# Kernel optimization log

Measured on AMD Instinct MI355X. Metric: run time of the kernel, lower is better.

Reference implementation:

```python
import jax, jax.numpy as jnp
import numpy as np

N = [40000, 10000, 2500, 625, 157]  # vertex counts per mesh level (0 = full res)
K = 6


def _propagate(x, row, col, norm, n):
    # x: [B, N_in, C]; gather neighbor feats, weight by norm, scatter-add to rows
    msg = x[:, col, :] * norm[None, :, None]          # [B, E, C]
    return jnp.zeros((x.shape[0], n, x.shape[2]), x.dtype).at[:, row, :].add(msg)


def cheb_conv(x, edge_index, W, b, n):
    # Chebyshev graph conv with sym-normalized adjacency (lambda_max=2 / CoMA convention)
    row, col = edge_index[0], edge_index[1]
    deg = jnp.zeros((n,), x.dtype).at[row].add(jnp.ones(row.shape, x.dtype))
    dinv = jnp.where(deg > 0, deg ** -0.5, jnp.zeros_like(deg))
    norm = dinv[row] * dinv[col]
    Tx0 = x
    out = jnp.einsum('bnc,cd->bnd', Tx0, W[0])
    Tx1 = _propagate(Tx0, row, col, norm, n)
    out = out + jnp.einsum('bnc,cd->bnd', Tx1, W[1])
    for k in range(2, W.shape[0]):
        Tx2 = 2.0 * _propagate(Tx1, row, col, norm, n) - Tx0
        out = out + jnp.einsum('bnc,cd->bnd', Tx2, W[k])
        Tx0, Tx1 = Tx1, Tx2
    return out + b


def pool(x, row, col, val, n_out):
    # sparse COO upsampling: out[:, row] += val * x[:, col]  (Pool() in torch source)
    msg = x[:, col, :] * val[None, :, None]
    return jnp.zeros((x.shape[0], n_out, x.shape[2]), x.dtype).at[:, row, :].add(msg)


def setup_inputs() -> dict:
    key = jax.random.key(0)
    ks = iter(jax.random.split(key, 64))
    B, latent = 16, 128
    inp = {}
    inp['x'] = jax.random.normal(next(ks), (B, latent), jnp.float32)
    inp['lin_w'] = jax.random.normal(next(ks), (latent, N[4] * 64), jnp.float32) * 0.05
    inp['lin_b'] = jnp.zeros((N[4] * 64,), jnp.float32)
    for i in range(4):
        inp[f'edge{i}'] = jax.random.randint(next(ks), (2, 6 * N[i]), 0, N[i])
    for i in range(4):
        nnz = 3 * N[i]
        inp[f'up{i}_row'] = jax.random.randint(next(ks), (nnz,), 0, N[i])
        inp[f'up{i}_col'] = jax.random.randint(next(ks), (nnz,), 0, N[i + 1])
        inp[f'up{i}_val'] = jax.random.uniform(next(ks), (nnz,), jnp.float32)
    # Deblock Cheb weights: (in,out) = (64,64),(64,32),(32,32),(32,32); final (32,3)
    for j, (ci, co) in enumerate([(64, 64), (64, 32), (32, 32), (32, 32)], start=1):
        inp[f'W{j}'] = jax.random.normal(next(ks), (K, ci, co), jnp.float32) * 0.05
        inp[f'b{j}'] = jnp.zeros((co,), jnp.float32)
    inp['Wout'] = jax.random.normal(next(ks), (K, 32, 3), jnp.float32) * 0.05
    inp['bout'] = jnp.zeros((3,), jnp.float32)
    return inp


def reference(x, lin_w, lin_b, edge0, edge1, edge2, edge3,
              up0_row, up0_col, up0_val, up1_row, up1_col, up1_val,
              up2_row, up2_col, up2_val, up3_row, up3_col, up3_val,
              W1, b1, W2, b2, W3, b3, W4, b4, Wout, bout):
    B = x.shape[0]
    h = (x @ lin_w + lin_b).reshape(B, N[4], 64)        # latent -> coarsest mesh
    edges = [edge0, edge1, edge2, edge3]
    ups = [(up0_row, up0_col, up0_val), (up1_row, up1_col, up1_val),
           (up2_row, up2_col, up2_val), (up3_row, up3_col, up3_val)]
    Ws = [(W1, b1), (W2, b2), (W3, b3), (W4, b4)]
    for j in range(4):
        lvl = 3 - j  # deblock j upsamples to mesh level lvl (coarse -> fine)
        row, col, val = ups[lvl]
        h = pool(h, row, col, val, N[lvl])
        h = jax.nn.elu(cheb_conv(h, edges[lvl], Ws[j][0], Ws[j][1], N[lvl]))
    return cheb_conv(h, edge0, Wout, bout, N[0])        # [B, 40000, 3]
```

## Files before the change

### kernel.cpp

```cpp
#include <hip/hip_runtime.h>
#include <math.h>

#define TB 256
#define SCAN_TOT 106250
#define SCAN_NB  104

typedef __bf16 bf16x8 __attribute__((ext_vector_type(8)));
typedef float f32x4 __attribute__((ext_vector_type(4)));
typedef float f32x2 __attribute__((ext_vector_type(2)));

static __device__ __forceinline__ int gtid() { return blockIdx.x * blockDim.x + threadIdx.x; }

static __device__ __forceinline__ void fma4(float4& a, float s, const float4 b) {
  a.x = fmaf(s, b.x, a.x); a.y = fmaf(s, b.y, a.y);
  a.z = fmaf(s, b.z, a.z); a.w = fmaf(s, b.w, a.w);
}

static __device__ __forceinline__ float bfus(unsigned short u) {
  union { unsigned u; float f; } c; c.u = ((unsigned)u) << 16; return c.f;
}
static __device__ __forceinline__ unsigned f2bf(float f) {
  union { float f; unsigned u; } c; c.f = f;
  return (c.u + 0x7fffu + ((c.u >> 16) & 1u)) >> 16;
}
static __device__ __forceinline__ unsigned pk2(float a, float b) {
  return f2bf(a) | (f2bf(b) << 16);
}
static __device__ __forceinline__ f32x2 unpk(unsigned u) {
  union { unsigned u; float f; } lo, hi;
  lo.u = u << 16; hi.u = u & 0xffff0000u;
  f32x2 r; r.x = lo.f; r.y = hi.f; return r;
}

__global__ void fill_kernel(float* __restrict__ p, int n, float v) {
  int i = gtid(); if (i < n) p[i] = v;
}

__global__ void zero_int_kernel(int* __restrict__ p, int n) {
  int i = gtid(); if (i < n) p[i] = 0;
}

struct SegD {
  const int* rows[8];
  const int* cols[8];
  const float* vals[8];
  int start[8];
  int degb[8];
};

__global__ void count_all_kernel(SegD sg, int total, int* __restrict__ deg) {
  int t = gtid(); if (t >= total) return;
  int seg = 0;
  #pragma unroll
  for (int q = 1; q < 8; ++q) seg += (t >= sg.start[q]);
  int i = t - sg.start[seg];
  atomicAdd(&deg[sg.degb[seg] + sg.rows[seg][i]], 1);
}

__global__ void fill_all_kernel(SegD sg, int total, const int* __restrict__ deg,
                                const int* __restrict__ offs, int* __restrict__ cursor,
                                int* __restrict__ ccol, float* __restrict__ cwa) {
  int t = gtid(); if (t >= total) return;
  int seg = 0;
  #pragma unroll
  for (int q = 1; q < 8; ++q) seg += (t >= sg.start[q]);
  int i = t - sg.start[seg];
  int db = sg.degb[seg];
  int r = sg.rows[seg][i];
  int c = sg.cols[seg][i];
  int p = atomicAdd(&cursor[db + r], 1);
  int idx = offs[db + r] + p;
  float w;
  if (sg.vals[seg]) {
    w = sg.vals[seg][i];
  } else {
    int dc = deg[db + c];
    w = rsqrtf((float)deg[db + r]) * (dc > 0 ? rsqrtf((float)dc) : 0.f);
  }
  ccol[idx] = c;
  cwa[idx] = w;
}

__global__ void scan_phase1(const int* __restrict__ in, int* __restrict__ bsum) {
  __shared__ int wsum[4];
  int blk = blockIdx.x, t = threadIdx.x;
  int base = blk * 1024 + t * 4;
  int s = 0;
  #pragma unroll
  for (int q = 0; q < 4; ++q) { int i = base + q; if (i < SCAN_TOT) s += in[i]; }
  #pragma unroll
  for (int o = 32; o > 0; o >>= 1) s += __shfl_xor(s, o, 64);
  int lane = t & 63, wid = t >> 6;
  if (lane == 0) wsum[wid] = s;
  __syncthreads();
  if (t == 0) bsum[blk] = wsum[0] + wsum[1] + wsum[2] + wsum[3];
}

__global__ void scan_phase2(int* __restrict__ bsum, int* __restrict__ offs_end) {
  int t = threadIdx.x;
  int v = (t < SCAN_NB) ? bsum[t] : 0;
  int lane = t & 63, wid = t >> 6;
  int p = v;
  #pragma unroll
  for (int o = 1; o < 64; o <<= 1) { int u = __shfl_up(p, o, 64); if (lane >= o) p += u; }
  __shared__ int w0tot;
  if (wid == 0 && lane == 63) w0tot = p;
  __syncthreads();
  int incl = p + (wid ? w0tot : 0);
  if (t < SCAN_NB) bsum[t] = incl - v;
  if (t == 127) offs_end[0] = incl;
}

__global__ void scan_phase3(const int* __restrict__ in, const int* __restrict__ bbase,
                            int* __restrict__ offs, int* __restrict__ cursor) {
  __shared__ int wsum[4];
  int blk = blockIdx.x, t = threadIdx.x;
  int base = blk * 1024 + t * 4;
  int v[4]; int s = 0;
  #pragma unroll
  for (int q = 0; q < 4; ++q) { int i = base + q; v[q] = (i < SCAN_TOT) ? in[i] : 0; s += v[q]; }
  int lane = t & 63, wid = t >> 6;
  int p = s;
  #pragma unroll
  for (int o = 1; o < 64; o <<= 1) { int u = __shfl_up(p, o, 64); if (lane >= o) p += u; }
  if (lane == 63) wsum[wid] = p;
  __syncthreads();
  int woff = 0;
  #pragma unroll
  for (int q = 0; q < 4; ++q) woff += (q < wid) ? wsum[q] : 0;
  int ex = bbase[blk] + woff + p - s;
  #pragma unroll
  for (int q = 0; q < 4; ++q) {
    int i = base + q;
    if (i < SCAN_TOT) { offs[i] = ex; cursor[i] = 0; ex += v[q]; }
  }
}

__global__ void wconv_kernel(const float* __restrict__ W, unsigned* __restrict__ Wt) {
  int p = gtid();
  if (p >= 6 * 32 * 16) return;
  int kk2 = p & 15;
  int col = (p >> 4) & 31;
  int kidx = p >> 9;
  float v0 = W[kidx * 1024 + (2 * kk2) * 32 + col];
  float v1 = W[kidx * 1024 + (2 * kk2 + 1) * 32 + col];
  Wt[(kidx * 32 + col) * 16 + kk2] = pk2(v0, v1);
}

__global__ void pool_kernel(const float4* __restrict__ x, const int* __restrict__ offs,
                            const int* __restrict__ ccol, const float* __restrict__ cw,
                            float4* __restrict__ out, int n, int xs4, int xoff4,
                            int os4, int osh) {
  int t = gtid();
  if (t >= n * os4) return;
  int v = t >> osh, j = t & (os4 - 1);
  int s = offs[v], e = offs[v + 1];
  float4 a = {0.f, 0.f, 0.f, 0.f};
  for (int i = s; i < e; ++i)
    fma4(a, cw[i], x[(long long)ccol[i] * xs4 + xoff4 + j]);
  out[t] = a;
}

__global__ void pool_f2b_kernel(const float4* __restrict__ x, const int* __restrict__ offs,
                                const int* __restrict__ ccol, const float* __restrict__ cw,
                                uint4* __restrict__ out, int n) {
  int t = gtid();
  if (t >= n * 64) return;
  int v = t >> 6, j = t & 63;
  int s = offs[v], e = offs[v + 1];
  float4 a0 = {0.f, 0.f, 0.f, 0.f}, a1 = {0.f, 0.f, 0.f, 0.f};
  for (int i = s; i < e; ++i) {
    float w = cw[i];
    const float4* xr = x + (long long)ccol[i] * 128 + j * 2;
    fma4(a0, w, xr[0]); fma4(a1, w, xr[1]);
  }
  uint4 r;
  r.x = pk2(a0.x, a0.y); r.y = pk2(a0.z, a0.w);
  r.z = pk2(a1.x, a1.y); r.w = pk2(a1.z, a1.w);
  out[t] = r;
}

__global__ void pool_b2b_kernel(const uint4* __restrict__ x, const int* __restrict__ offs,
                                const int* __restrict__ ccol, const float* __restrict__ cw,
                                uint4* __restrict__ out, int n) {
  int t = gtid();
  if (t >= n * 64) return;
  int v = t >> 6, j = t & 63;
  int s = offs[v], e = offs[v + 1];
  f32x2 a0 = {0.f, 0.f}, a1 = {0.f, 0.f}, a2 = {0.f, 0.f}, a3 = {0.f, 0.f};
  for (int i = s; i < e; ++i) {
    float w = cw[i];
    f32x2 w2 = {w, w};
    uint4 xv = x[(long long)ccol[i] * 64 + j];
    a0 = __builtin_elementwise_fma(w2, unpk(xv.x), a0);
    a1 = __builtin_elementwise_fma(w2, unpk(xv.y), a1);
    a2 = __builtin_elementwise_fma(w2, unpk(xv.z), a2);
    a3 = __builtin_elementwise_fma(w2, unpk(xv.w), a3);
  }
  uint4 r;
  r.x = pk2(a0.x, a0.y); r.y = pk2(a1.x, a1.y);
  r.z = pk2(a2.x, a2.y); r.w = pk2(a3.x, a3.y);
  out[t] = r;
}

template<int CIN, int COUT>
__global__ void cheb_step_kernel(const float* __restrict__ X,
                                 const float* __restrict__ b1,
                                 float* __restrict__ b2o,
                                 const float* __restrict__ Wk,
                                 const float* __restrict__ bias,
                                 const int* __restrict__ offs,
                                 const int* __restrict__ ccol,
                                 const float* __restrict__ cw,
                                 int n, int LB, int mode) {
  constexpr int CS = COUT / 8;
  constexpr int LCS = (CS == 8) ? 3 : 2;
  constexpr int W4 = COUT / 4;
  __shared__ float sW[CIN * COUT];
  for (int i = threadIdx.x; i < CIN * COUT; i += blockDim.x) sW[i] = Wk[i];
  __syncthreads();
  int t = gtid();
  int BI = 1 << LB;
  if (t >= n * BI * CS) return;
  int cs = t & (CS - 1);
  int r = t >> LCS;
  int v = r >> LB;
  int bi = r & (BI - 1);
  float4 a0 = {0.f, 0.f, 0.f, 0.f}, a1 = {0.f, 0.f, 0.f, 0.f};
  const float4* Xr = (const float4*)(X + (long long)r * CIN);
  const float4* wbase = ((const float4*)sW) + cs * 2;
  #pragma unroll
  for (int c4 = 0; c4 < CIN / 4; ++c4) {
    float4 xv = Xr[c4];
    const float4* w = wbase + (c4 * 4) * W4;
    fma4(a0, xv.x, w[0]); fma4(a1, xv.x, w[1]); w += W4;
    fma4(a0, xv.y, w[0]); fma4(a1, xv.y, w[1]); w += W4;
    fma4(a0, xv.z, w[0]); fma4(a1, xv.z, w[1]); w += W4;
    fma4(a0, xv.w, w[0]); fma4(a1, xv.w, w[1]);
  }
  if (mode >= 1) {
    float sc = (mode == 3) ? 1.f : 2.f;
    int s = offs[v], e = offs[v + 1];
    const float4* b14 = (const float4*)b1;
    for (int i = s; i < e; ++i) {
      float w = cw[i] * sc;
      long long rb = (long long)((ccol[i] << LB) | bi) * W4 + cs * 2;
      fma4(a0, w, b14[rb]); fma4(a1, w, b14[rb + 1]);
    }
  }
  float4* Or = ((float4*)b2o) + (long long)r * W4 + cs * 2;
  if (mode >= 2) {
    float4 p0 = Or[0], p1 = Or[1];
    a0.x -= p0.x; a0.y -= p0.y; a0.z -= p0.z; a0.w -= p0.w;
    a1.x -= p1.x; a1.y -= p1.y; a1.z -= p1.z; a1.w -= p1.w;
  }
  if (mode == 3) {
    const float* bs = bias + cs * 8;
    a0.x += bs[0]; a0.y += bs[1]; a0.z += bs[2]; a0.w += bs[3];
    a1.x += bs[4]; a1.y += bs[5]; a1.z += bs[6]; a1.w += bs[7];
    a0.x = a0.x > 0.f ? a0.x : expm1f(a0.x);
    a0.y = a0.y > 0.f ? a0.y : expm1f(a0.y);
    a0.z = a0.z > 0.f ? a0.z : expm1f(a0.z);
    a0.w = a0.w > 0.f ? a0.w : expm1f(a0.w);
    a1.x = a1.x > 0.f ? a1.x : expm1f(a1.x);
    a1.y = a1.y > 0.f ? a1.y : expm1f(a1.y);
    a1.z = a1.z > 0.f ? a1.z : expm1f(a1.z);
    a1.w = a1.w > 0.f ? a1.w : expm1f(a1.w);
  }
  Or[0] = a0; Or[1] = a1;
}

__global__ void __launch_bounds__(256)
cheb_mfma32_kernel(const uint4* __restrict__ X,
                   const unsigned* __restrict__ b1,
                   unsigned* __restrict__ b2o,
                   const uint4* __restrict__ Wtk,
                   const float* __restrict__ bias,
                   const int* __restrict__ offs,
                   const int* __restrict__ ccol,
                   const float* __restrict__ cw,
                   int n, int mode) {
  int lane = threadIdx.x & 63;
  int v = (blockIdx.x << 2) | (threadIdx.x >> 6);
  if (v >= n) return;
  int g = lane >> 4;
  int c15 = lane & 15;

  union { uint4 u; bf16x8 b; } Au, B0u, B1u;
  Au.u = X[((long long)(v * 16 + c15)) * 4 + g];
  B0u.u = Wtk[c15 * 4 + g];
  B1u.u = Wtk[(16 + c15) * 4 + g];

  f32x4 z = {0.f, 0.f, 0.f, 0.f};
  f32x4 m0 = __builtin_amdgcn_mfma_f32_16x16x32_bf16(Au.b, B0u.b, z, 0, 0, 0);
  f32x4 m1 = __builtin_amdgcn_mfma_f32_16x16x32_bf16(Au.b, B1u.b, z, 0, 0, 0);
  f32x2 acc[4];
  #pragma unroll
  for (int q = 0; q < 4; ++q) { acc[q].x = m0[q]; acc[q].y = m1[q]; }

  long long own = (long long)v * 256 + 64 * g + c15;
  if (mode >= 1) {
    float sc = (mode == 3) ? 1.f : 2.f;
    int s = offs[v], e = offs[v + 1];
    for (int i = s; i < e; ++i) {
      float w = cw[i] * sc;
      f32x2 w2 = {w, w};
      long long base = (long long)ccol[i] * 256 + 64 * g + c15;
      #pragma unroll
      for (int q = 0; q < 4; ++q)
        acc[q] = __builtin_elementwise_fma(w2, unpk(b1[base + 16 * q]), acc[q]);
    }
  }
  if (mode >= 2) {
    #pragma unroll
    for (int q = 0; q < 4; ++q)
      acc[q] -= unpk(b2o[own + 16 * q]);
  }
  if (mode == 3) {
    float bs0 = bias[c15], bs1 = bias[16 + c15];
    unsigned short* o = (unsigned short*)b2o;
    long long lb = ((long long)v * 16 + 4 * g) * 32;
    #pragma unroll
    for (int q = 0; q < 4; ++q) {
      float a = acc[q].x + bs0;
      float b = acc[q].y + bs1;
      a = a > 0.f ? a : expm1f(a);
      b = b > 0.f ? b : expm1f(b);
      o[lb + q * 32 + c15] = (unsigned short)f2bf(a);
      o[lb + q * 32 + 16 + c15] = (unsigned short)f2bf(b);
    }
  } else {
    #pragma unroll
    for (int q = 0; q < 4; ++q)
      b2o[own + 16 * q] = pk2(acc[q].x, acc[q].y);
  }
}

__global__ void gemm_out_all_kernel(const uint4* __restrict__ X, const float* __restrict__ W,
                                    unsigned short* __restrict__ c_all, int nr) {
  __shared__ float sW[576];
  for (int i = threadIdx.x; i < 576; i += blockDim.x) sW[i] = W[i];
  __syncthreads();
  int r = gtid();
  if (r >= nr) return;
  const uint4* Xr = X + (long long)r * 4;
  float xa[32];
  #pragma unroll
  for (int q = 0; q < 4; ++q) {
    uint4 xv = Xr[q];
    f32x2 p0 = unpk(xv.x), p1 = unpk(xv.y), p2 = unpk(xv.z), p3 = unpk(xv.w);
    xa[q * 8 + 0] = p0.x; xa[q * 8 + 1] = p0.y;
    xa[q * 8 + 2] = p1.x; xa[q * 8 + 3] = p1.y;
    xa[q * 8 + 4] = p2.x; xa[q * 8 + 5] = p2.y;
    xa[q * 8 + 6] = p3.x; xa[q * 8 + 7] = p3.y;
  }
  float acc[18];
  #pragma unroll
  for (int i = 0; i < 18; ++i) acc[i] = 0.f;
  #pragma unroll
  for (int c = 0; c < 32; ++c) {
    float xc = xa[c];
    #pragma unroll
    for (int k = 0; k < 6; ++k) {
      acc[k * 3 + 0] = fmaf(xc, sW[k * 96 + c * 3 + 0], acc[k * 3 + 0]);
      acc[k * 3 + 1] = fmaf(xc, sW[k * 96 + c * 3 + 1], acc[k * 3 + 1]);
      acc[k * 3 + 2] = fmaf(xc, sW[k * 96 + c * 3 + 2], acc[k * 3 + 2]);
    }
  }
  #pragma unroll
  for (int k = 0; k < 6; ++k) {
    unsigned short* o = c_all + ((long long)k * nr + r) * 3;
    o[0] = (unsigned short)f2bf(acc[k * 3 + 0]);
    o[1] = (unsigned short)f2bf(acc[k * 3 + 1]);
    o[2] = (unsigned short)f2bf(acc[k * 3 + 2]);
  }
}

__global__ void cheb_out_step_kernel(const unsigned short* __restrict__ c_all, int k,
                                     const float* __restrict__ b1,
                                     float* __restrict__ b2o,
                                     const float* __restrict__ bias,
                                     const int* __restrict__ offs,
                                     const int* __restrict__ ccol,
                                     const float* __restrict__ cw,
                                     int n, float* __restrict__ dout, int mode) {
  int r = gtid();
  if (r >= n * 16) return;
  int v = r >> 4, bi = r & 15;
  const unsigned short* cr = c_all + ((long long)k * n * 16 + r) * 3;
  float a0 = bfus(cr[0]), a1 = bfus(cr[1]), a2 = bfus(cr[2]);
  if (mode >= 1) {
    float sc = (mode == 3) ? 1.f : 2.f;
    int s = offs[v], e = offs[v + 1];
    for (int i = s; i < e; ++i) {
      float w = cw[i] * sc;
      const float* br = b1 + (long long)((ccol[i] << 4) | bi) * 3;
      a0 = fmaf(w, br[0], a0); a1 = fmaf(w, br[1], a1); a2 = fmaf(w, br[2], a2);
    }
  }
  if (mode >= 2) {
    const float* p = b2o + (long long)r * 3;
    a0 -= p[0]; a1 -= p[1]; a2 -= p[2];
  }
  if (mode == 3) {
    a0 += bias[0]; a1 += bias[1]; a2 += bias[2];
    float* o = dout + ((long long)bi * n + v) * 3;
    o[0] = a0; o[1] = a1; o[2] = a2;
  } else {
    float* o = b2o + (long long)r * 3;
    o[0] = a0; o[1] = a1; o[2] = a2;
  }
}

__global__ void linear_kernel(const float* __restrict__ x, const float* __restrict__ w,
                              const float* __restrict__ bias, float* __restrict__ out) {
  int t = gtid();
  const int TOT = 157 * 16 * 64;
  if (t >= TOT) return;
  int c = t & 63;
  int b = (t >> 6) & 15;
  int v = t >> 10;
  int colw = v * 64 + c;
  float acc = bias[colw];
  const float* xr = x + b * 128;
  for (int k = 0; k < 128; ++k) acc = fmaf(xr[k], w[k * 10048 + colw], acc);
  out[t] = acc;
}

extern "C" void kernel_launch(void* const* d_in, const int* in_sizes, int n_in,
                              void* d_out, int out_size, void* d_ws, size_t ws_size,
                              hipStream_t stream) {
  const int N[4] = {40000, 10000, 2500, 625};
  const int E[4] = {240000, 60000, 15000, 3750};
  const int NNZ[4] = {120000, 30000, 7500, 1875};
  const int DP[4] = {0, 40000, 50000, 52500};
  const int DE[4] = {53125, 93125, 103125, 105625};
  const int ITEMS = 478125;

  const float* x     = (const float*)d_in[0];
  const float* lin_w = (const float*)d_in[1];
  const float* lin_b = (const float*)d_in[2];
  const int* edge[4] = {(const int*)d_in[3], (const int*)d_in[4], (const int*)d_in[5], (const int*)d_in[6]};
  const int* up_row[4]; const int* up_col[4]; const float* up_val[4];
  for (int i = 0; i < 4; ++i) {
    up_row[i] = (const int*)d_in[7 + 3 * i];
    up_col[i] = (const int*)d_in[8 + 3 * i];
    up_val[i] = (const float*)d_in[9 + 3 * i];
  }
  const float* W_[5] = {(const float*)d_in[19], (const float*)d_in[21], (const float*)d_in[23],
                        (const float*)d_in[25], (const float*)d_in[27]};
  const float* b_[5] = {(const float*)d_in[20], (const float*)d_in[22], (const float*)d_in[24],
                        (const float*)d_in[26], (const float*)d_in[28]};

  char* ws = (char*)d_ws;
  size_t off = 0;
  auto alloc = [&](size_t bytes) -> void* {
    void* p = ws + off;
    off = (off + bytes + 255) & ~(size_t)255;
    return p;
  };
  auto cdiv = [](int a, int b) { return (a + b - 1) / b; };

  float* slot[4];
  for (int i = 0; i < 4; ++i) slot[i] = (float*)alloc(20480000ull);
  uint4* Ab = (uint4*)alloc(40960000ull);
  unsigned* Bb = (unsigned*)alloc(40960000ull);
  unsigned* Cb = (unsigned*)alloc(40960000ull);
  unsigned short* c_all = (unsigned short*)alloc((size_t)6 * 640000 * 3 * 2);
  float* ob1 = (float*)alloc((size_t)640000 * 3 * 4);
  float* ob2 = (float*)alloc((size_t)640000 * 3 * 4);
  int* deg_all    = (int*)alloc(SCAN_TOT * 4);
  int* cursor_all = (int*)alloc(SCAN_TOT * 4);
  int* offs_all   = (int*)alloc((SCAN_TOT + 1) * 4);
  int* bsum       = (int*)alloc(SCAN_NB * 4);
  int* col_arena  = (int*)alloc((size_t)ITEMS * 4);
  float* w_arena  = (float*)alloc((size_t)ITEMS * 4);
  uint4* Wt2 = (uint4*)alloc(6 * 128 * 16);
  uint4* Wt3 = (uint4*)alloc(6 * 128 * 16);

  if (off > ws_size) {
    fill_kernel<<<cdiv(out_size, TB), TB, 0, stream>>>((float*)d_out, out_size,
                                                       (float)(ws_size >> 20));
    return;
  }

  SegD sg;
  int cum = 0;
  for (int l = 0; l < 4; ++l) {
    sg.rows[l] = up_row[l]; sg.cols[l] = up_col[l]; sg.vals[l] = up_val[l];
    sg.start[l] = cum; sg.degb[l] = DP[l]; cum += NNZ[l];
  }
  for (int l = 0; l < 4; ++l) {
    sg.rows[4 + l] = edge[l]; sg.cols[4 + l] = edge[l] + E[l]; sg.vals[4 + l] = nullptr;
    sg.start[4 + l] = cum; sg.degb[4 + l] = DE[l]; cum += E[l];
  }
  zero_int_kernel<<<cdiv(SCAN_TOT, TB), TB, 0, stream>>>(deg_all, SCAN_TOT);
  count_all_kernel<<<cdiv(ITEMS, TB), TB, 0, stream>>>(sg, ITEMS, deg_all);
  scan_phase1<<<SCAN_NB, TB, 0, stream>>>(deg_all, bsum);
  scan_phase2<<<1, 128, 0, stream>>>(bsum, offs_all + SCAN_TOT);
  scan_phase3<<<SCAN_NB, TB, 0, stream>>>(deg_all, bsum, offs_all, cursor_all);
  fill_all_kernel<<<cdiv(ITEMS, TB), TB, 0, stream>>>(sg, ITEMS, deg_all, offs_all,
                                                      cursor_all, col_arena, w_arena);
  wconv_kernel<<<cdiv(3072, TB), TB, 0, stream>>>(W_[2], (unsigned*)Wt2);
  wconv_kernel<<<cdiv(3072, TB), TB, 0, stream>>>(W_[3], (unsigned*)Wt3);

  linear_kernel<<<cdiv(157 * 16 * 64, TB), TB, 0, stream>>>(x, lin_w, lin_b, slot[0]);
  float* H = slot[0];
  float* A = slot[1];
  float* B = slot[2];
  float* C = slot[3];

  const int CINA[2]  = {64, 64};
  const int COUTA[2] = {64, 32};

  for (int j = 0; j < 2; ++j) {
    int lvl = 3 - j;
    int n = N[lvl];
    int cin = CINA[j], cout = COUTA[j];
    int os4 = 16 * cin / 4;
    int osh = (os4 == 256) ? 8 : 7;
    const int* offs_p = offs_all + DP[lvl];
    const int* offs_e = offs_all + DE[lvl];

    pool_kernel<<<cdiv(n * os4, TB), TB, 0, stream>>>(
        (const float4*)H, offs_p, col_arena, w_arena, (float4*)A, n, os4, 0, os4, osh);

    int cs = cout / 8;
    dim3 g(cdiv(n * 16 * cs, TB));
    auto step = [&](const float* b1, float* b2o, int k, int mode) {
      const float* Wk = W_[j] + (size_t)k * cin * cout;
      if (cin == 64 && cout == 64)
        hipLaunchKernelGGL((cheb_step_kernel<64, 64>), g, dim3(TB), 0, stream,
                           A, b1, b2o, Wk, b_[j], offs_e, col_arena, w_arena, n, 4, mode);
      else
        hipLaunchKernelGGL((cheb_step_kernel<64, 32>), g, dim3(TB), 0, stream,
                           A, b1, b2o, Wk, b_[j], offs_e, col_arena, w_arena, n, 4, mode);
    };
    step(nullptr, B, 5, 0);
    step(B, C, 4, 1);
    step(C, B, 3, 2);
    step(B, C, 2, 2);
    step(C, B, 1, 2);
    step(B, C, 0, 3);

    float* tmp = H; H = C; C = tmp;
  }
  float* freeA = A;
  float* freeB = B;
  float* freeC = C;

  uint4* Ab1 = (uint4*)freeA;
  unsigned* Bb1 = (unsigned*)freeB;
  unsigned* Cb1 = (unsigned*)freeC;
  {
    int n = N[1];
    pool_f2b_kernel<<<cdiv(n * 64, TB), TB, 0, stream>>>(
        (const float4*)H, offs_all + DP[1], col_arena, w_arena, Ab1, n);
    dim3 gmf(n / 4);
    auto dstep = [&](const unsigned* b1, unsigned* b2o, int k, int mode) {
      cheb_mfma32_kernel<<<gmf, dim3(256), 0, stream>>>(
          Ab1, b1, b2o, Wt2 + (size_t)k * 128, b_[2],
          offs_all + DE[1], col_arena, w_arena, n, mode);
    };
    dstep(nullptr, Bb1, 5, 0);
    dstep(Bb1, Cb1, 4, 1);
    dstep(Cb1, Bb1, 3, 2);
    dstep(Bb1, Cb1, 2, 2);
    dstep(Cb1, Bb1, 1, 2);
    dstep(Bb1, Cb1, 0, 3);
  }

  {
    int n = N[0];
    int nr = n * 16;
    const int* offs_e = offs_all + DE[0];

    pool_b2b_kernel<<<cdiv(n * 64, TB), TB, 0, stream>>>(
        (const uint4*)Cb1, offs_all + DP[0], col_arena, w_arena, Ab, n);

    dim3 gmf(n / 4);
    auto dstep = [&](const unsigned* b1, unsigned* b2o, int k, int mode) {
      cheb_mfma32_kernel<<<gmf, dim3(256), 0, stream>>>(
          Ab, b1, b2o, Wt3 + (size_t)k * 128, b_[3],
          offs_e, col_arena, w_arena, n, mode);
    };
    dstep(nullptr, Bb, 5, 0);
    dstep(Bb, Cb, 4, 1);
    dstep(Cb, Bb, 3, 2);
    dstep(Bb, Cb, 2, 2);
    dstep(Cb, Bb, 1, 2);
    dstep(Bb, Cb, 0, 3);

    dim3 gr(cdiv(nr, TB));
    gemm_out_all_kernel<<<gr, dim3(TB), 0, stream>>>((const uint4*)Cb, W_[4], c_all, nr);
    float* dout = (float*)d_out;
    auto ostep = [&](const float* b1, float* b2o, int k, int mode) {
      cheb_out_step_kernel<<<gr, dim3(TB), 0, stream>>>(
          c_all, k, b1, b2o, b_[4], offs_e, col_arena, w_arena, n, dout, mode);
    };
    ostep(nullptr, ob1, 5, 0);
    ostep(ob1, ob2, 4, 1);
    ostep(ob2, ob1, 3, 2);
    ostep(ob1, ob2, 2, 2);
    ostep(ob2, ob1, 1, 2);
    ostep(ob1, ob2, 0, 3);
  }
}
```

Baseline: 766.1 us.

## Fuse pooling with first Chebyshev MFMA step and vectorize bf16 intermediate layout

Pooling for the two finest levels now runs in an MFMA-style kernel that writes the pooled bf16 features and also computes the k=5 weight product, so the separate mode-0 Chebyshev launch is removed. The intermediate buffers are reordered so each lane reads and writes one 16-byte uint4 per neighbor instead of four scattered 4-byte words. Manual bf16 rounding is replaced with the native __bf16 conversion. The change saves a launch and a re-read of the pooled features and coalesces the gathers. The cost is a pool kernel that must match the MFMA lane mapping, and the new permuted layout has to stay consistent across all consumers.

```diff
diff --git a/kernel.cpp b/kernel.cpp
--- a/kernel.cpp
+++ b/kernel.cpp
@@ -19,12 +19,13 @@
 static __device__ __forceinline__ float bfus(unsigned short u) {
   union { unsigned u; float f; } c; c.u = ((unsigned)u) << 16; return c.f;
 }
-static __device__ __forceinline__ unsigned f2bf(float f) {
-  union { float f; unsigned u; } c; c.f = f;
-  return (c.u + 0x7fffu + ((c.u >> 16) & 1u)) >> 16;
-}
 static __device__ __forceinline__ unsigned pk2(float a, float b) {
-  return f2bf(a) | (f2bf(b) << 16);
+  union { unsigned u; __bf16 h[2]; } c;
+  c.h[0] = (__bf16)a; c.h[1] = (__bf16)b;
+  return c.u;
+}
+static __device__ __forceinline__ unsigned short us1(float a) {
+  union { unsigned short u; __bf16 h; } c; c.h = (__bf16)a; return c.u;
 }
 static __device__ __forceinline__ f32x2 unpk(unsigned u) {
   union { unsigned u; float f; } lo, hi;
@@ -161,46 +162,60 @@
   out[t] = a;
 }
 
-__global__ void pool_f2b_kernel(const float4* __restrict__ x, const int* __restrict__ offs,
-                                const int* __restrict__ ccol, const float* __restrict__ cw,
-                                uint4* __restrict__ out, int n) {
-  int t = gtid();
-  if (t >= n * 64) return;
-  int v = t >> 6, j = t & 63;
+template<int SRC>
+__global__ void __launch_bounds__(256)
+pool_mfma_kernel(const void* __restrict__ xsrc, const int* __restrict__ offs,
+                 const int* __restrict__ ccol, const float* __restrict__ cw,
+                 uint4* __restrict__ Xout, uint4* __restrict__ b5out,
+                 const uint4* __restrict__ Wtk5, int n) {
+  int lane = threadIdx.x & 63;
+  int v = (blockIdx.x << 2) | (threadIdx.x >> 6);
+  if (v >= n) return;
+  int g = lane >> 4, c15 = lane & 15;
   int s = offs[v], e = offs[v + 1];
-  float4 a0 = {0.f, 0.f, 0.f, 0.f}, a1 = {0.f, 0.f, 0.f, 0.f};
-  for (int i = s; i < e; ++i) {
-    float w = cw[i];
-    const float4* xr = x + (long long)ccol[i] * 128 + j * 2;
-    fma4(a0, w, xr[0]); fma4(a1, w, xr[1]);
-  }
-  uint4 r;
-  r.x = pk2(a0.x, a0.y); r.y = pk2(a0.z, a0.w);
-  r.z = pk2(a1.x, a1.y); r.w = pk2(a1.z, a1.w);
-  out[t] = r;
-}
-
-__global__ void pool_b2b_kernel(const uint4* __restrict__ x, const int* __restrict__ offs,
-                                const int* __restrict__ ccol, const float* __restrict__ cw,
-                                uint4* __restrict__ out, int n) {
-  int t = gtid();
-  if (t >= n * 64) return;
-  int v = t >> 6, j = t & 63;
-  int s = offs[v], e = offs[v + 1];
-  f32x2 a0 = {0.f, 0.f}, a1 = {0.f, 0.f}, a2 = {0.f, 0.f}, a3 = {0.f, 0.f};
-  for (int i = s; i < e; ++i) {
-    float w = cw[i];
-    f32x2 w2 = {w, w};
-    uint4 xv = x[(long long)ccol[i] * 64 + j];
-    a0 = __builtin_elementwise_fma(w2, unpk(xv.x), a0);
-    a1 = __builtin_elementwise_fma(w2, unpk(xv.y), a1);
-    a2 = __builtin_elementwise_fma(w2, unpk(xv.z), a2);
-    a3 = __builtin_elementwise_fma(w2, unpk(xv.w), a3);
-  }
-  uint4 r;
-  r.x = pk2(a0.x, a0.y); r.y = pk2(a1.x, a1.y);
-  r.z = pk2(a2.x, a2.y); r.w = pk2(a3.x, a3.y);
-  out[t] = r;
+  float a[8];
+  #pragma unroll
+  for (int q = 0; q < 8; ++q) a[q] = 0.f;
+  if (SRC == 0) {
+    const float4* x = (const float4*)xsrc;
+    for (int i = s; i < e; ++i) {
+      float w = cw[i];
+      const float4* xr = x + (long long)ccol[i] * 128 + c15 * 8 + g * 2;
+      float4 x0 = xr[0], x1 = xr[1];
+      a[0] = fmaf(w, x0.x, a[0]); a[1] = fmaf(w, x0.y, a[1]);
+      a[2] = fmaf(w, x0.z, a[2]); a[3] = fmaf(w, x0.w, a[3]);
+      a[4] = fmaf(w, x1.x, a[4]); a[5] = fmaf(w, x1.y, a[5]);
+      a[6] = fmaf(w, x1.z, a[6]); a[7] = fmaf(w, x1.w, a[7]);
+    }
+  } else {
+    const uint4* x = (const uint4*)xsrc;
+    for (int i = s; i < e; ++i) {
+      float w = cw[i];
+      f32x2 w2 = {w, w};
+      uint4 xv = x[(long long)ccol[i] * 64 + c15 * 4 + g];
+      f32x2 p0 = __builtin_elementwise_fma(w2, unpk(xv.x), f32x2{a[0], a[1]});
+      f32x2 p1 = __builtin_elementwise_fma(w2, unpk(xv.y), f32x2{a[2], a[3]});
+      f32x2 p2 = __builtin_elementwise_fma(w2, unpk(xv.z), f32x2{a[4], a[5]});
+      f32x2 p3 = __builtin_elementwise_fma(w2, unpk(xv.w), f32x2{a[6], a[7]});
+      a[0] = p0.x; a[1] = p0.y; a[2] = p1.x; a[3] = p1.y;
+      a[4] = p2.x; a[5] = p2.y; a[6] = p3.x; a[7] = p3.y;
+    }
+  }
+  union { uint4 u; bf16x8 b; } Au;
+  Au.u.x = pk2(a[0], a[1]); Au.u.y = pk2(a[2], a[3]);
+  Au.u.z = pk2(a[4], a[5]); Au.u.w = pk2(a[6], a[7]);
+  Xout[(long long)v * 64 + c15 * 4 + g] = Au.u;
+
+  union { uint4 u; bf16x8 b; } B0u, B1u;
+  B0u.u = Wtk5[c15 * 4 + g];
+  B1u.u = Wtk5[(16 + c15) * 4 + g];
+  f32x4 z = {0.f, 0.f, 0.f, 0.f};
+  f32x4 m0 = __builtin_amdgcn_mfma_f32_16x16x32_bf16(Au.b, B0u.b, z, 0, 0, 0);
+  f32x4 m1 = __builtin_amdgcn_mfma_f32_16x16x32_bf16(Au.b, B1u.b, z, 0, 0, 0);
+  uint4 o;
+  o.x = pk2(m0[0], m1[0]); o.y = pk2(m0[1], m1[1]);
+  o.z = pk2(m0[2], m1[2]); o.w = pk2(m0[3], m1[3]);
+  b5out[(long long)v * 64 + g * 16 + c15] = o;
 }
 
 template<int CIN, int COUT>
@@ -272,8 +287,8 @@
 
 __global__ void __launch_bounds__(256)
 cheb_mfma32_kernel(const uint4* __restrict__ X,
-                   const unsigned* __restrict__ b1,
-                   unsigned* __restrict__ b2o,
+                   const uint4* __restrict__ b1,
+                   uint4* __restrict__ b2o,
                    const uint4* __restrict__ Wtk,
                    const float* __restrict__ bias,
                    const int* __restrict__ offs,
@@ -287,7 +302,7 @@
   int c15 = lane & 15;
 
   union { uint4 u; bf16x8 b; } Au, B0u, B1u;
-  Au.u = X[((long long)(v * 16 + c15)) * 4 + g];
+  Au.u = X[(long long)v * 64 + c15 * 4 + g];
   B0u.u = Wtk[c15 * 4 + g];
   B1u.u = Wtk[(16 + c15) * 4 + g];
 
@@ -298,23 +313,24 @@
   #pragma unroll
   for (int q = 0; q < 4; ++q) { acc[q].x = m0[q]; acc[q].y = m1[q]; }
 
-  long long own = (long long)v * 256 + 64 * g + c15;
+  long long own = (long long)v * 64 + g * 16 + c15;
   if (mode >= 1) {
     float sc = (mode == 3) ? 1.f : 2.f;
     int s = offs[v], e = offs[v + 1];
     for (int i = s; i < e; ++i) {
       float w = cw[i] * sc;
       f32x2 w2 = {w, w};
-      long long base = (long long)ccol[i] * 256 + 64 * g + c15;
-      #pragma unroll
-      for (int q = 0; q < 4; ++q)
-        acc[q] = __builtin_elementwise_fma(w2, unpk(b1[base + 16 * q]), acc[q]);
+      uint4 bv = b1[(long long)ccol[i] * 64 + g * 16 + c15];
+      acc[0] = __builtin_elementwise_fma(w2, unpk(bv.x), acc[0]);
+      acc[1] = __builtin_elementwise_fma(w2, unpk(bv.y), acc[1]);
+      acc[2] = __builtin_elementwise_fma(w2, unpk(bv.z), acc[2]);
+      acc[3] = __builtin_elementwise_fma(w2, unpk(bv.w), acc[3]);
     }
   }
   if (mode >= 2) {
-    #pragma unroll
-    for (int q = 0; q < 4; ++q)
-      acc[q] -= unpk(b2o[own + 16 * q]);
+    uint4 pv = b2o[own];
+    acc[0] -= unpk(pv.x); acc[1] -= unpk(pv.y);
+    acc[2] -= unpk(pv.z); acc[3] -= unpk(pv.w);
   }
   if (mode == 3) {
     float bs0 = bias[c15], bs1 = bias[16 + c15];
@@ -326,13 +342,14 @@
       float b = acc[q].y + bs1;
       a = a > 0.f ? a : expm1f(a);
       b = b > 0.f ? b : expm1f(b);
-      o[lb + q * 32 + c15] = (unsigned short)f2bf(a);
-      o[lb + q * 32 + 16 + c15] = (unsigned short)f2bf(b);
+      o[lb + q * 32 + c15] = us1(a);
+      o[lb + q * 32 + 16 + c15] = us1(b);
     }
   } else {
-    #pragma unroll
-    for (int q = 0; q < 4; ++q)
-      b2o[own + 16 * q] = pk2(acc[q].x, acc[q].y);
+    uint4 o;
+    o.x = pk2(acc[0].x, acc[0].y); o.y = pk2(acc[1].x, acc[1].y);
+    o.z = pk2(acc[2].x, acc[2].y); o.w = pk2(acc[3].x, acc[3].y);
+    b2o[own] = o;
   }
 }
 
@@ -370,9 +387,9 @@
   #pragma unroll
   for (int k = 0; k < 6; ++k) {
     unsigned short* o = c_all + ((long long)k * nr + r) * 3;
-    o[0] = (unsigned short)f2bf(acc[k * 3 + 0]);
-    o[1] = (unsigned short)f2bf(acc[k * 3 + 1]);
-    o[2] = (unsigned short)f2bf(acc[k * 3 + 2]);
+    o[0] = us1(acc[k * 3 + 0]);
+    o[1] = us1(acc[k * 3 + 1]);
+    o[2] = us1(acc[k * 3 + 2]);
   }
 }
 
@@ -464,8 +481,8 @@
   float* slot[4];
   for (int i = 0; i < 4; ++i) slot[i] = (float*)alloc(20480000ull);
   uint4* Ab = (uint4*)alloc(40960000ull);
-  unsigned* Bb = (unsigned*)alloc(40960000ull);
-  unsigned* Cb = (unsigned*)alloc(40960000ull);
+  uint4* Bb = (uint4*)alloc(40960000ull);
+  uint4* Cb = (uint4*)alloc(40960000ull);
   unsigned short* c_all = (unsigned short*)alloc((size_t)6 * 640000 * 3 * 2);
   float* ob1 = (float*)alloc((size_t)640000 * 3 * 4);
   float* ob2 = (float*)alloc((size_t)640000 * 3 * 4);
@@ -550,19 +567,19 @@
   float* freeC = C;
 
   uint4* Ab1 = (uint4*)freeA;
-  unsigned* Bb1 = (unsigned*)freeB;
-  unsigned* Cb1 = (unsigned*)freeC;
+  uint4* Bb1 = (uint4*)freeB;
+  uint4* Cb1 = (uint4*)freeC;
   {
     int n = N[1];
-    pool_f2b_kernel<<<cdiv(n * 64, TB), TB, 0, stream>>>(
-        (const float4*)H, offs_all + DP[1], col_arena, w_arena, Ab1, n);
     dim3 gmf(n / 4);
-    auto dstep = [&](const unsigned* b1, unsigned* b2o, int k, int mode) {
+    hipLaunchKernelGGL((pool_mfma_kernel<0>), gmf, dim3(256), 0, stream,
+                       (const void*)H, offs_all + DP[1], col_arena, w_arena,
+                       Ab1, Bb1, Wt2 + (size_t)5 * 128, n);
+    auto dstep = [&](const uint4* b1, uint4* b2o, int k, int mode) {
       cheb_mfma32_kernel<<<gmf, dim3(256), 0, stream>>>(
           Ab1, b1, b2o, Wt2 + (size_t)k * 128, b_[2],
           offs_all + DE[1], col_arena, w_arena, n, mode);
     };
-    dstep(nullptr, Bb1, 5, 0);
     dstep(Bb1, Cb1, 4, 1);
     dstep(Cb1, Bb1, 3, 2);
     dstep(Bb1, Cb1, 2, 2);
@@ -574,17 +591,17 @@
     int n = N[0];
     int nr = n * 16;
     const int* offs_e = offs_all + DE[0];
-
-    pool_b2b_kernel<<<cdiv(n * 64, TB), TB, 0, stream>>>(
-        (const uint4*)Cb1, offs_all + DP[0], col_arena, w_arena, Ab, n);
-
     dim3 gmf(n / 4);
-    auto dstep = [&](const unsigned* b1, unsigned* b2o, int k, int mode) {
+
+    hipLaunchKernelGGL((pool_mfma_kernel<1>), gmf, dim3(256), 0, stream,
+                       (const void*)Cb1, offs_all + DP[0], col_arena, w_arena,
+                       Ab, Bb, Wt3 + (size_t)5 * 128, n);
+
+    auto dstep = [&](const uint4* b1, uint4* b2o, int k, int mode) {
       cheb_mfma32_kernel<<<gmf, dim3(256), 0, stream>>>(
           Ab, b1, b2o, Wt3 + (size_t)k * 128, b_[3],
           offs_e, col_arena, w_arena, n, mode);
     };
-    dstep(nullptr, Bb, 5, 0);
     dstep(Bb, Cb, 4, 1);
     dstep(Cb, Bb, 3, 2);
     dstep(Bb, Cb, 2, 2);
```

Result: no change. 759.4 us (-0.9%).
